# Optimization experiments

Measured on AMD Instinct MI355X. Metric: run time of the kernel, lower is better.

## Reference

```python
import jax, jax.numpy as jnp
import numpy as np

B, H, W, C, HEADS = 4, 64, 64, 512, 8
HD = C // HEADS
L = H * W
BIAS_LEVEL = 0.1
LN_EPS = 1e-5


def _ln(x, g, b):
    mu = jnp.mean(x, axis=-1, keepdims=True)
    var = jnp.var(x, axis=-1, keepdims=True)
    return (x - mu) * jax.lax.rsqrt(var + LN_EPS) * g + b


def setup_inputs() -> dict:
    key = jax.random.key(0)
    ks = jax.random.split(key, 16)
    s = 0.02
    return {
        "x": jax.random.normal(ks[0], (B, L, C), jnp.float32),
        "rpe": jax.random.normal(ks[1], (H, HEADS, W, W), jnp.float32),
        "qkv_w": jax.random.normal(ks[2], (3 * C, C), jnp.float32) * s,
        "proj_w": jax.random.normal(ks[3], (C, C), jnp.float32) * s,
        "proj_b": jnp.zeros((C,), jnp.float32),
        "norm1_w": jnp.ones((C,), jnp.float32),
        "norm1_b": jnp.zeros((C,), jnp.float32),
        "norm2_w": jnp.ones((C,), jnp.float32),
        "norm2_b": jnp.zeros((C,), jnp.float32),
        "fc1_w": jax.random.normal(ks[4], (4 * C, C), jnp.float32) * s,
        "fc1_b": jnp.zeros((4 * C,), jnp.float32),
        "fc2_w": jax.random.normal(ks[5], (C, 4 * C), jnp.float32) * s,
        "fc2_b": jnp.zeros((C,), jnp.float32),
    }


def reference(x, rpe, qkv_w, proj_w, proj_b, norm1_w, norm1_b, norm2_w, norm2_b,
              fc1_w, fc1_b, fc2_w, fc2_b):
    # --- qkv projection ---
    img = _ln(x, norm1_w, norm1_b)
    qkv = (img @ qkv_w.T).reshape(B, L, 3, C)
    q, k, v = qkv[:, :, 0], qkv[:, :, 1], qkv[:, :, 2]

    # idx=0 horizontal windows: each row of the HxW grid is a window of len W.
    def to_win(t):  # (B, L, C) -> (B*H, heads, W, hd)
        return t.reshape(B * H, W, HEADS, HD).transpose(0, 2, 1, 3)

    qw, kw, vw = to_win(q), to_win(k), to_win(v)

    # attention scores + relative position bias (RPE tiled over batch)
    attn = jnp.einsum('whqd,whkd->whqk', qw, kw)
    attn = attn + BIAS_LEVEL * jnp.tile(rpe, (B, 1, 1, 1))

    # magnitude gate M per window
    M = jnp.mean(jnp.abs(attn), axis=(1, 2, 3), keepdims=True)  # (B*H,1,1,1)
    M = M / jnp.max(M)
    M = jnp.maximum(M, 0.5)

    # cosine-based score transform: 1 - cos(pi/2 * l2normalize(attn))
    nrm = jnp.maximum(jnp.linalg.norm(attn, axis=-1, keepdims=True), 1e-12)
    attn = 1.0 - jnp.cos((attn / nrm) * (jnp.pi / 2.0))
    attn = attn * M

    o = jnp.einsum('whqk,whkd->whqd', attn, vw)  # (B*H, heads, W, hd)
    o = o.transpose(0, 2, 1, 3).reshape(B, L, C)

    # residual gating by (1 - M)
    res = (x.reshape(B * H, 1, W, C) * (1.0 - M)).reshape(B, L, C)
    attened = o + res

    attened = attened @ proj_w.T + proj_b
    x1 = x + attened

    h = _ln(x1, norm2_w, norm2_b)
    h = jax.nn.gelu(h @ fc1_w.T + fc1_b, approximate=False)
    h = h @ fc2_w.T + fc2_b
    return x1 + h
```

## Files before the change

### kernel.cpp

```cpp
#include <hip/hip_runtime.h>
#include <hip/hip_bf16.h>
#include <math.h>

typedef unsigned short u16;
typedef __bf16 bf16x8 __attribute__((ext_vector_type(8)));
typedef float f32x4 __attribute__((ext_vector_type(4)));
typedef unsigned short u16x8 __attribute__((ext_vector_type(8)));

typedef const __attribute__((address_space(1))) void* gas_ptr;
typedef __attribute__((address_space(3))) void* las_ptr;

__device__ __forceinline__ float bf2f(u16 u) {
    union { unsigned int i; float f; } x;
    x.i = ((unsigned int)u) << 16;
    return x.f;
}
__device__ __forceinline__ u16 f2bf(float f) {
    __hip_bfloat16 h = __float2bfloat16(f);
    return __builtin_bit_cast(u16, h);
}
__device__ __forceinline__ __bf16 f2bfr(float f) {
    __hip_bfloat16 h = __float2bfloat16(f);
    return __builtin_bit_cast(__bf16, h);
}
__device__ __forceinline__ void load_lds16(const void* g, void* l) {
    __builtin_amdgcn_global_load_lds((gas_ptr)g, (las_ptr)l, 16, 0, 0);
}

__global__ __launch_bounds__(256) void cvt_k(const float* __restrict__ in,
                                             u16* __restrict__ outp) {
    const int i = blockIdx.x * 256 + threadIdx.x;
    const float4 v = ((const float4*)in)[i];
    ushort4 o;
    o.x = f2bf(v.x); o.y = f2bf(v.y); o.z = f2bf(v.z); o.w = f2bf(v.w);
    ((ushort4*)outp)[i] = o;
}

__global__ __launch_bounds__(256) void ln_k(const float* __restrict__ inp,
                                            const float* __restrict__ gw,
                                            const float* __restrict__ gb,
                                            u16* __restrict__ outp) {
    const int row = blockIdx.x, t = threadIdx.x;
    const float2 v = ((const float2*)(inp + (size_t)row * 512))[t];
    float s = v.x + v.y, q = v.x * v.x + v.y * v.y;
    #pragma unroll
    for (int o = 1; o < 64; o <<= 1) {
        s += __shfl_xor(s, o);
        q += __shfl_xor(q, o);
    }
    __shared__ float rs[4], rq[4];
    const int w = t >> 6;
    if ((t & 63) == 0) { rs[w] = s; rq[w] = q; }
    __syncthreads();
    s = rs[0] + rs[1] + rs[2] + rs[3];
    q = rq[0] + rq[1] + rq[2] + rq[3];
    const float mean = s * (1.0f / 512.0f);
    const float var = q * (1.0f / 512.0f) - mean * mean;
    const float rstd = rsqrtf(var + 1e-5f);
    u16* op = outp + (size_t)row * 512;
    op[2 * t]     = f2bf((v.x - mean) * rstd * gw[2 * t]     + gb[2 * t]);
    op[2 * t + 1] = f2bf((v.y - mean) * rstd * gw[2 * t + 1] + gb[2 * t + 1]);
}

template<int EPI>
__global__ __launch_bounds__(256) void gemm_bt(const u16* __restrict__ A,
                                               const u16* __restrict__ W,
                                               const float* __restrict__ bias,
                                               const float* __restrict__ res_f,
                                               void* __restrict__ outp,
                                               int M, int N, int K) {
    __shared__ __bf16 As[2][128 * 32];
    __shared__ __bf16 Bs[2][128 * 32];
    const int t = threadIdx.x;
    const int l = t & 63;
    const int w = t >> 6;
    const int wm = w & 1, wn = w >> 1;
    const int bm = blockIdx.x * 128, bn = blockIdx.y * 128;

    f32x4 acc[4][4] = {};

    auto stage = [&](int buf, int kt) {
        #pragma unroll
        for (int p = 0; p < 2; ++p) {
            const int sb = (p * 256 + t) << 4;
            const int row = sb >> 6;
            const int gl = ((sb >> 4) & 3) ^ (row & 3);
            const int lbase = p * 2048 + w * 512;
            load_lds16(A + (size_t)(bm + row) * K + kt + gl * 8, &As[buf][lbase]);
            load_lds16(W + (size_t)(bn + row) * K + kt + gl * 8, &Bs[buf][lbase]);
        }
    };

    const int nk = K >> 5;
    stage(0, 0);
    __syncthreads();
    for (int s = 0; s < nk; ++s) {
        if (s + 1 < nk) stage((s + 1) & 1, (s + 1) << 5);
        const int buf = s & 1;
        const int r = l & 15, g = l >> 4;
        bf16x8 af[4], bfr[4];
        #pragma unroll
        for (int i = 0; i < 4; ++i) {
            const int ra = wm * 64 + i * 16 + r;
            af[i] = *(const bf16x8*)&As[buf][ra * 32 + ((g ^ (ra & 3)) << 3)];
            const int rb = wn * 64 + i * 16 + r;
            bfr[i] = *(const bf16x8*)&Bs[buf][rb * 32 + ((g ^ (rb & 3)) << 3)];
        }
        #pragma unroll
        for (int i = 0; i < 4; ++i)
            #pragma unroll
            for (int j = 0; j < 4; ++j)
                acc[i][j] = __builtin_amdgcn_mfma_f32_16x16x32_bf16(af[i], bfr[j], acc[i][j], 0, 0, 0);
        __syncthreads();
    }

    #pragma unroll
    for (int i = 0; i < 4; ++i) {
        #pragma unroll
        for (int j = 0; j < 4; ++j) {
            #pragma unroll
            for (int rr = 0; rr < 4; ++rr) {
                const int m = bm + wm * 64 + i * 16 + ((l >> 4) << 2) + rr;
                const int n = bn + wn * 64 + j * 16 + (l & 15);
                float v = acc[i][j][rr];
                const size_t idx = (size_t)m * N + n;
                if (EPI == 0) {
                    ((u16*)outp)[idx] = f2bf(v);
                } else if (EPI == 1) {
                    ((float*)outp)[idx] = v + bias[n] + res_f[idx];
                } else {
                    v += bias[n];
                    v = 0.5f * v * (1.0f + erff(v * 0.70710678118654752f));
                    ((u16*)outp)[idx] = f2bf(v);
                }
            }
        }
    }
}

__global__ __launch_bounds__(256) void attn_k(const u16* __restrict__ qkv,
                                              const float* __restrict__ rpe,
                                              float* __restrict__ Mpart,
                                              u16* __restrict__ Obuf) {
    const int blk = blockIdx.x;
    const int wh = blk >> 3, head = blk & 7;
    const int himg = wh & 63;
    const int t = threadIdx.x, l = t & 63, w = t >> 6;
    __shared__ __bf16 Qs[4096];
    __shared__ __bf16 Ks[4096];
    __shared__ __bf16 Vt[4096];
    __shared__ __bf16 Ps[4096];
    __shared__ float red[4];

    #pragma unroll
    for (int p = 0; p < 2; ++p) {
        const int sb = (p * 256 + t) << 4;
        const int row = sb >> 7;
        const int gl = ((sb >> 4) & 7) ^ (row & 7);
        const size_t gsrc = (size_t)(wh * 64 + row) * 1536 + head * 64 + gl * 8;
        const int lbase = p * 2048 + w * 512;
        load_lds16(qkv + gsrc, &Qs[lbase]);
        load_lds16(qkv + gsrc + 512, &Ks[lbase]);
    }
    {
        const int k = t >> 2, dc = (t & 3) * 16;
        const u16* vr = qkv + (size_t)(wh * 64 + k) * 1536 + 1024 + head * 64 + dc;
        u16x8 v0 = *(const u16x8*)vr;
        u16x8 v1 = *(const u16x8*)(vr + 8);
        const int g = k >> 3, klo = k & 7;
        #pragma unroll
        for (int i = 0; i < 8; ++i) {
            const int d0 = dc + i, d1 = dc + 8 + i;
            Vt[d0 * 64 + ((g ^ (d0 & 7)) << 3) + klo] = __builtin_bit_cast(__bf16, (u16)v0[i]);
            Vt[d1 * 64 + ((g ^ (d1 & 7)) << 3) + klo] = __builtin_bit_cast(__bf16, (u16)v1[i]);
        }
    }
    __syncthreads();

    const int r = l & 15, g4 = l >> 4;
    f32x4 acc[4] = {};
    #pragma unroll
    for (int h = 0; h < 2; ++h) {
        const int rowq = w * 16 + r;
        bf16x8 aq = *(const bf16x8*)&Qs[rowq * 64 + (((h * 4 + g4) ^ (rowq & 7)) << 3)];
        #pragma unroll
        for (int j = 0; j < 4; ++j) {
            const int rowk = j * 16 + r;
            bf16x8 bk = *(const bf16x8*)&Ks[rowk * 64 + (((h * 4 + g4) ^ (rowk & 7)) << 3)];
            acc[j] = __builtin_amdgcn_mfma_f32_16x16x32_bf16(aq, bk, acc[j], 0, 0, 0);
        }
    }

    float v[4][4];
    float asum = 0.f;
    float ss[4] = {0.f, 0.f, 0.f, 0.f};
    const size_t rpe_base = (size_t)(himg * 8 + head) * 4096 + (size_t)(w * 16 + g4 * 4) * 64 + r;
    #pragma unroll
    for (int j = 0; j < 4; ++j) {
        #pragma unroll
        for (int rr = 0; rr < 4; ++rr) {
            const float val = acc[j][rr] + 0.1f * rpe[rpe_base + rr * 64 + j * 16];
            v[j][rr] = val;
            asum += fabsf(val);
            ss[rr] += val * val;
        }
    }
    #pragma unroll
    for (int m = 1; m < 16; m <<= 1) {
        #pragma unroll
        for (int rr = 0; rr < 4; ++rr) ss[rr] += __shfl_xor(ss[rr], m);
    }
    float srev[4];
    #pragma unroll
    for (int rr = 0; rr < 4; ++rr)
        srev[rr] = 0.25f / fmaxf(sqrtf(ss[rr]), 1e-12f);

    #pragma unroll
    for (int j = 0; j < 4; ++j) {
        #pragma unroll
        for (int rr = 0; rr < 4; ++rr) {
            const float pv = 1.0f - __builtin_amdgcn_cosf(v[j][rr] * srev[rr]);
            const int rl = g4 * 4 + rr;
            const int c = j * 16 + r;
            Ps[w * 1024 + rl * 64 + (((c >> 3) ^ (rl & 7)) << 3) + (c & 7)] = f2bfr(pv);
        }
    }

    f32x4 oacc[4] = {};
    #pragma unroll
    for (int ks = 0; ks < 2; ++ks) {
        const int ga = ks * 4 + g4;
        bf16x8 pa = *(const bf16x8*)&Ps[w * 1024 + r * 64 + ((ga ^ (r & 7)) << 3)];
        #pragma unroll
        for (int j = 0; j < 4; ++j) {
            const int d = j * 16 + r;
            bf16x8 vb = *(const bf16x8*)&Vt[d * 64 + ((ga ^ (d & 7)) << 3)];
            oacc[j] = __builtin_amdgcn_mfma_f32_16x16x32_bf16(pa, vb, oacc[j], 0, 0, 0);
        }
    }

    #pragma unroll
    for (int j = 0; j < 4; ++j) {
        #pragma unroll
        for (int rr = 0; rr < 4; ++rr) {
            const int token = wh * 64 + w * 16 + g4 * 4 + rr;
            Obuf[(size_t)token * 512 + head * 64 + j * 16 + r] = f2bf(oacc[j][rr]);
        }
    }

    #pragma unroll
    for (int o = 1; o < 64; o <<= 1) asum += __shfl_xor(asum, o);
    if (l == 0) red[w] = asum;
    __syncthreads();
    if (t == 0) Mpart[blk] = red[0] + red[1] + red[2] + red[3];
}

__global__ __launch_bounds__(256) void mfinal_k(const float* __restrict__ Mpart,
                                                float* __restrict__ M) {
    const int t = threadIdx.x;
    float m = 0.f;
    #pragma unroll
    for (int h = 0; h < 8; ++h) m += Mpart[t * 8 + h];
    m *= (1.0f / 32768.0f);
    float mx = m;
    #pragma unroll
    for (int o = 1; o < 64; o <<= 1) mx = fmaxf(mx, __shfl_xor(mx, o));
    __shared__ float red[4];
    if ((t & 63) == 0) red[t >> 6] = mx;
    __syncthreads();
    mx = fmaxf(fmaxf(red[0], red[1]), fmaxf(red[2], red[3]));
    M[t] = fmaxf(m / mx, 0.5f);
}

__global__ __launch_bounds__(256) void a1_k(const u16* __restrict__ O,
                                            const float* __restrict__ M,
                                            const float* __restrict__ x,
                                            u16* __restrict__ A1) {
    const size_t i8 = ((size_t)blockIdx.x * 256 + threadIdx.x) * 8;
    const float Mw = M[i8 >> 15];
    const float rf = 1.0f - Mw;
    const u16x8 ov = *(const u16x8*)(O + i8);
    const float4 x0 = *(const float4*)(x + i8);
    const float4 x1 = *(const float4*)(x + i8 + 4);
    u16x8 res;
    res[0] = f2bf(bf2f(ov[0]) * Mw + x0.x * rf);
    res[1] = f2bf(bf2f(ov[1]) * Mw + x0.y * rf);
    res[2] = f2bf(bf2f(ov[2]) * Mw + x0.z * rf);
    res[3] = f2bf(bf2f(ov[3]) * Mw + x0.w * rf);
    res[4] = f2bf(bf2f(ov[4]) * Mw + x1.x * rf);
    res[5] = f2bf(bf2f(ov[5]) * Mw + x1.y * rf);
    res[6] = f2bf(bf2f(ov[6]) * Mw + x1.z * rf);
    res[7] = f2bf(bf2f(ov[7]) * Mw + x1.w * rf);
    *(u16x8*)(A1 + i8) = res;
}

extern "C" void kernel_launch(void* const* d_in, const int* in_sizes, int n_in,
                              void* d_out, int out_size, void* d_ws, size_t ws_size,
                              hipStream_t stream) {
    (void)in_sizes; (void)n_in; (void)out_size; (void)ws_size;
    const float* x      = (const float*)d_in[0];
    const float* rpe    = (const float*)d_in[1];
    const float* qkv_w  = (const float*)d_in[2];
    const float* proj_w = (const float*)d_in[3];
    const float* proj_b = (const float*)d_in[4];
    const float* n1w    = (const float*)d_in[5];
    const float* n1b    = (const float*)d_in[6];
    const float* n2w    = (const float*)d_in[7];
    const float* n2b    = (const float*)d_in[8];
    const float* fc1w   = (const float*)d_in[9];
    const float* fc1b   = (const float*)d_in[10];
    const float* fc2w   = (const float*)d_in[11];
    const float* fc2b   = (const float*)d_in[12];
    float* out = (float*)d_out;

    char* ws = (char*)d_ws;
    float* Mpart = (float*)ws;
    float* Mbuf  = (float*)(ws + 8192);
    u16* wqkv  = (u16*)(ws + 16384);
    u16* wproj = (u16*)(ws + 16384 + 1572864);
    u16* wfc1  = (u16*)(ws + 16384 + 2097152);
    u16* wfc2  = (u16*)(ws + 16384 + 4194304);
    u16* bufA  = (u16*)(ws + 6307840);
    char* R    = ws + 23085056;
    u16*   qkvb = (u16*)R;
    u16*   Obuf = (u16*)(R + 50331648);
    u16*   gbuf = (u16*)R;

    cvt_k<<<768, 256, 0, stream>>>(qkv_w, wqkv);
    cvt_k<<<256, 256, 0, stream>>>(proj_w, wproj);
    cvt_k<<<1024, 256, 0, stream>>>(fc1w, wfc1);
    cvt_k<<<1024, 256, 0, stream>>>(fc2w, wfc2);
    ln_k<<<16384, 256, 0, stream>>>(x, n1w, n1b, bufA);
    gemm_bt<0><<<dim3(128, 12), 256, 0, stream>>>(bufA, wqkv, nullptr, nullptr,
                                                  qkvb, 16384, 1536, 512);
    attn_k<<<2048, 256, 0, stream>>>(qkvb, rpe, Mpart, Obuf);
    mfinal_k<<<1, 256, 0, stream>>>(Mpart, Mbuf);
    a1_k<<<4096, 256, 0, stream>>>(Obuf, Mbuf, x, bufA);
    gemm_bt<1><<<dim3(128, 4), 256, 0, stream>>>(bufA, wproj, proj_b, x,
                                                 out, 16384, 512, 512);
    ln_k<<<16384, 256, 0, stream>>>(out, n2w, n2b, bufA);
    gemm_bt<2><<<dim3(128, 16), 256, 0, stream>>>(bufA, wfc1, fc1b, nullptr,
                                                  gbuf, 16384, 2048, 512);
    gemm_bt<1><<<dim3(128, 4), 256, 0, stream>>>(gbuf, wfc2, fc2b, out,
                                                 out, 16384, 512, 2048);
}
```

Measured before the change: 221.1 us.

## Replace GEMM with 8-wave 256-wide tiled kernel using phased LDS prefetch pipeline

Replaces the 128x128, 4-wave GEMM with a 512-thread kernel that computes 128x256 or 256x256 output tiles using K-steps of 64. Loads of A and B into LDS are split into halves and interleaved with MFMA quarters, separated by explicit barriers and vmcnt waits, with raised wave priority around the MFMA sections. The goal is better operand reuse per LDS load and overlap of global-to-LDS traffic with matrix math in all four GEMMs. In exchange it uses more registers and LDS per block, which lowers occupancy. The schedule also depends on hand-tuned wait counts whose correctness has to hold for every stage.

```diff
diff --git a/kernel.cpp b/kernel.cpp
--- a/kernel.cpp
+++ b/kernel.cpp
@@ -26,6 +26,12 @@
 __device__ __forceinline__ void load_lds16(const void* g, void* l) {
     __builtin_amdgcn_global_load_lds((gas_ptr)g, (las_ptr)l, 16, 0, 0);
 }
+__device__ __forceinline__ void phase_bar() {
+    __builtin_amdgcn_sched_barrier(0);
+    __builtin_amdgcn_s_barrier();
+    __builtin_amdgcn_sched_barrier(0);
+}
+#define VMCNT4() asm volatile("s_waitcnt vmcnt(4)" ::: "memory")
 
 __global__ __launch_bounds__(256) void cvt_k(const float* __restrict__ in,
                                              u16* __restrict__ outp) {
@@ -62,66 +68,122 @@
     op[2 * t + 1] = f2bf((v.y - mean) * rstd * gw[2 * t + 1] + gb[2 * t + 1]);
 }
 
-template<int EPI>
-__global__ __launch_bounds__(256) void gemm_bt(const u16* __restrict__ A,
-                                               const u16* __restrict__ W,
-                                               const float* __restrict__ bias,
-                                               const float* __restrict__ res_f,
-                                               void* __restrict__ outp,
-                                               int M, int N, int K) {
-    __shared__ __bf16 As[2][128 * 32];
-    __shared__ __bf16 Bs[2][128 * 32];
+template<int EPI, int M_REP>
+__global__ __launch_bounds__(512, 2) void gemm8(const u16* __restrict__ A,
+                                                const u16* __restrict__ W,
+                                                const float* __restrict__ bias,
+                                                const float* __restrict__ res_f,
+                                                void* __restrict__ outp,
+                                                int M, int N, int K) {
+    constexpr int BM  = M_REP * 32;
+    constexpr int IPQ = M_REP / 4;
+    constexpr int AL  = BM / 128;
+    __shared__ __bf16 As[2][BM * 64];
+    __shared__ __bf16 Bs[2][256 * 64];
     const int t = threadIdx.x;
     const int l = t & 63;
-    const int w = t >> 6;
-    const int wm = w & 1, wn = w >> 1;
-    const int bm = blockIdx.x * 128, bn = blockIdx.y * 128;
-
-    f32x4 acc[4][4] = {};
-
-    auto stage = [&](int buf, int kt) {
-        #pragma unroll
-        for (int p = 0; p < 2; ++p) {
-            const int sb = (p * 256 + t) << 4;
-            const int row = sb >> 6;
-            const int gl = ((sb >> 4) & 3) ^ (row & 3);
-            const int lbase = p * 2048 + w * 512;
-            load_lds16(A + (size_t)(bm + row) * K + kt + gl * 8, &As[buf][lbase]);
-            load_lds16(W + (size_t)(bn + row) * K + kt + gl * 8, &Bs[buf][lbase]);
+    const int wid = t >> 6;
+    const int wm = wid >> 2, wn = wid & 3;
+    const int bm = blockIdx.x * BM, bn = blockIdx.y * 256;
+    const int r = l & 15, g4 = l >> 4;
+    const int nk = K >> 6;
+    const int kmask = nk - 1;
+
+    f32x4 acc[M_REP][4] = {};
+    bf16x8 bfr[4][2];
+    bf16x8 af[IPQ][2];
+
+    auto stageA = [&](int buf, int h, int kt) __attribute__((always_inline)) {
+        const int k0 = (kt & kmask) << 6;
+        #pragma unroll
+        for (int j = 0; j < AL; ++j) {
+            const int gl = h * (BM * 4) + j * 512 + t;
+            const int row = gl >> 3, gc = gl & 7;
+            load_lds16(A + (size_t)(bm + row) * K + k0 + ((gc ^ (row & 7)) << 3),
+                       &As[buf][gl << 3]);
         }
     };
-
-    const int nk = K >> 5;
-    stage(0, 0);
-    __syncthreads();
-    for (int s = 0; s < nk; ++s) {
-        if (s + 1 < nk) stage((s + 1) & 1, (s + 1) << 5);
-        const int buf = s & 1;
-        const int r = l & 15, g = l >> 4;
-        bf16x8 af[4], bfr[4];
-        #pragma unroll
-        for (int i = 0; i < 4; ++i) {
-            const int ra = wm * 64 + i * 16 + r;
-            af[i] = *(const bf16x8*)&As[buf][ra * 32 + ((g ^ (ra & 3)) << 3)];
-            const int rb = wn * 64 + i * 16 + r;
-            bfr[i] = *(const bf16x8*)&Bs[buf][rb * 32 + ((g ^ (rb & 3)) << 3)];
-        }
-        #pragma unroll
-        for (int i = 0; i < 4; ++i)
+    auto stageB = [&](int buf, int h, int kt) __attribute__((always_inline)) {
+        const int k0 = (kt & kmask) << 6;
+        #pragma unroll
+        for (int j = 0; j < 2; ++j) {
+            const int gl = h * 1024 + j * 512 + t;
+            const int row = gl >> 3, gc = gl & 7;
+            load_lds16(W + (size_t)(bn + row) * K + k0 + ((gc ^ (row & 7)) << 3),
+                       &Bs[buf][gl << 3]);
+        }
+    };
+    auto dsB = [&](int buf) __attribute__((always_inline)) {
+        #pragma unroll
+        for (int j = 0; j < 4; ++j) {
+            #pragma unroll
+            for (int ks = 0; ks < 2; ++ks) {
+                const int row = wn * 64 + j * 16 + r;
+                const int gc = ks * 4 + g4;
+                bfr[j][ks] = *(const bf16x8*)&Bs[buf][((row << 3) | (gc ^ (row & 7))) << 3];
+            }
+        }
+    };
+    auto dsA = [&](int buf, int q) __attribute__((always_inline)) {
+        #pragma unroll
+        for (int ii = 0; ii < IPQ; ++ii) {
+            #pragma unroll
+            for (int ks = 0; ks < 2; ++ks) {
+                const int row = wm * (BM / 2) + (q * IPQ + ii) * 16 + r;
+                const int gc = ks * 4 + g4;
+                af[ii][ks] = *(const bf16x8*)&As[buf][((row << 3) | (gc ^ (row & 7))) << 3];
+            }
+        }
+    };
+    auto mfmaQ = [&](int q) __attribute__((always_inline)) {
+        __builtin_amdgcn_s_setprio(1);
+        #pragma unroll
+        for (int ii = 0; ii < IPQ; ++ii)
             #pragma unroll
             for (int j = 0; j < 4; ++j)
-                acc[i][j] = __builtin_amdgcn_mfma_f32_16x16x32_bf16(af[i], bfr[j], acc[i][j], 0, 0, 0);
-        __syncthreads();
-    }
-
-    #pragma unroll
-    for (int i = 0; i < 4; ++i) {
+                #pragma unroll
+                for (int ks = 0; ks < 2; ++ks)
+                    acc[q * IPQ + ii][j] = __builtin_amdgcn_mfma_f32_16x16x32_bf16(
+                        af[ii][ks], bfr[j][ks], acc[q * IPQ + ii][j], 0, 0, 0);
+        __builtin_amdgcn_s_setprio(0);
+    };
+
+    stageA(0, 0, 0); stageA(0, 1, 0);
+    stageB(0, 0, 0); stageB(0, 1, 0);
+    stageB(1, 0, 1); stageB(1, 1, 1);
+    VMCNT4();
+    phase_bar();
+
+    const int niter = nk >> 1;
+    for (int it = 0; it < niter; ++it) {
+        const int Ta = 2 * it;
+        dsB(0); dsA(0, 0);
+        stageA(1, 0, Ta + 1); stageA(1, 1, Ta + 1);
+        phase_bar(); mfmaQ(0); phase_bar();
+        dsA(0, 1); stageB(0, 0, Ta + 2);
+        phase_bar(); mfmaQ(1); phase_bar();
+        dsA(0, 2); stageB(0, 1, Ta + 2);
+        phase_bar(); mfmaQ(2); phase_bar();
+        dsA(0, 3); VMCNT4();
+        phase_bar(); mfmaQ(3); phase_bar();
+        dsB(1); dsA(1, 0); stageA(0, 0, Ta + 2);
+        phase_bar(); mfmaQ(0); phase_bar();
+        dsA(1, 1); stageA(0, 1, Ta + 2);
+        phase_bar(); mfmaQ(1); phase_bar();
+        dsA(1, 2); stageB(1, 0, Ta + 3);
+        phase_bar(); mfmaQ(2); phase_bar();
+        dsA(1, 3); stageB(1, 1, Ta + 3); VMCNT4();
+        phase_bar(); mfmaQ(3); phase_bar();
+    }
+
+    #pragma unroll
+    for (int i = 0; i < M_REP; ++i) {
         #pragma unroll
         for (int j = 0; j < 4; ++j) {
             #pragma unroll
             for (int rr = 0; rr < 4; ++rr) {
-                const int m = bm + wm * 64 + i * 16 + ((l >> 4) << 2) + rr;
-                const int n = bn + wn * 64 + j * 16 + (l & 15);
+                const int m = bm + wm * (BM / 2) + i * 16 + g4 * 4 + rr;
+                const int n = bn + wn * 64 + j * 16 + r;
                 float v = acc[i][j][rr];
                 const size_t idx = (size_t)m * N + n;
                 if (EPI == 0) {
@@ -331,16 +393,16 @@
     cvt_k<<<1024, 256, 0, stream>>>(fc1w, wfc1);
     cvt_k<<<1024, 256, 0, stream>>>(fc2w, wfc2);
     ln_k<<<16384, 256, 0, stream>>>(x, n1w, n1b, bufA);
-    gemm_bt<0><<<dim3(128, 12), 256, 0, stream>>>(bufA, wqkv, nullptr, nullptr,
-                                                  qkvb, 16384, 1536, 512);
+    gemm8<0, 8><<<dim3(64, 6), 512, 0, stream>>>(bufA, wqkv, nullptr, nullptr,
+                                                 qkvb, 16384, 1536, 512);
     attn_k<<<2048, 256, 0, stream>>>(qkvb, rpe, Mpart, Obuf);
     mfinal_k<<<1, 256, 0, stream>>>(Mpart, Mbuf);
     a1_k<<<4096, 256, 0, stream>>>(Obuf, Mbuf, x, bufA);
-    gemm_bt<1><<<dim3(128, 4), 256, 0, stream>>>(bufA, wproj, proj_b, x,
-                                                 out, 16384, 512, 512);
+    gemm8<1, 4><<<dim3(128, 2), 512, 0, stream>>>(bufA, wproj, proj_b, x,
+                                                  out, 16384, 512, 512);
     ln_k<<<16384, 256, 0, stream>>>(out, n2w, n2b, bufA);
-    gemm_bt<2><<<dim3(128, 16), 256, 0, stream>>>(bufA, wfc1, fc1b, nullptr,
-                                                  gbuf, 16384, 2048, 512);
-    gemm_bt<1><<<dim3(128, 4), 256, 0, stream>>>(gbuf, wfc2, fc2b, out,
-                                                 out, 16384, 512, 2048);
-}
+    gemm8<2, 8><<<dim3(64, 8), 512, 0, stream>>>(bufA, wfc1, fc1b, nullptr,
+                                                 gbuf, 16384, 2048, 512);
+    gemm8<1, 4><<<dim3(128, 2), 512, 0, stream>>>(gbuf, wfc2, fc2b, out,
+                                                  out, 16384, 512, 2048);
+}
```

Measured after the change: 229.1 us. 3.6% more time.

## Fuse attention residual gating into proj GEMM loader and store x1 as bf16

Applied to the files above, without the earlier changes.

Removes the standalone a1_k pass by computing M*O + (1-M)*x inside the proj GEMM's A-tile staging, writing the blended bf16 values straight to LDS. The proj output x1 is now stored as bf16 rather than fp32; LN2 reads it as bf16 and the final fc2 GEMM takes it as a bf16 residual. This cuts a full elementwise kernel and its traffic, and halves x1 read/write bytes, at the cost of synchronous register loads instead of async global_load_lds for the A tile and lower precision in the residual path.

```diff
diff --git a/kernel.cpp b/kernel.cpp
--- a/kernel.cpp
+++ b/kernel.cpp
@@ -36,13 +36,21 @@
     ((ushort4*)outp)[i] = o;
 }
 
-__global__ __launch_bounds__(256) void ln_k(const float* __restrict__ inp,
+template<bool BF16IN>
+__global__ __launch_bounds__(256) void ln_k(const void* __restrict__ inp,
                                             const float* __restrict__ gw,
                                             const float* __restrict__ gb,
                                             u16* __restrict__ outp) {
     const int row = blockIdx.x, t = threadIdx.x;
-    const float2 v = ((const float2*)(inp + (size_t)row * 512))[t];
-    float s = v.x + v.y, q = v.x * v.x + v.y * v.y;
+    float v0, v1;
+    if (BF16IN) {
+        const u16* rp = (const u16*)inp + (size_t)row * 512;
+        v0 = bf2f(rp[2 * t]); v1 = bf2f(rp[2 * t + 1]);
+    } else {
+        const float2 v = ((const float2*)((const float*)inp + (size_t)row * 512))[t];
+        v0 = v.x; v1 = v.y;
+    }
+    float s = v0 + v1, q = v0 * v0 + v1 * v1;
     #pragma unroll
     for (int o = 1; o < 64; o <<= 1) {
         s += __shfl_xor(s, o);
@@ -58,17 +66,21 @@
     const float var = q * (1.0f / 512.0f) - mean * mean;
     const float rstd = rsqrtf(var + 1e-5f);
     u16* op = outp + (size_t)row * 512;
-    op[2 * t]     = f2bf((v.x - mean) * rstd * gw[2 * t]     + gb[2 * t]);
-    op[2 * t + 1] = f2bf((v.y - mean) * rstd * gw[2 * t + 1] + gb[2 * t + 1]);
-}
-
-template<int EPI>
+    op[2 * t]     = f2bf((v0 - mean) * rstd * gw[2 * t]     + gb[2 * t]);
+    op[2 * t + 1] = f2bf((v1 - mean) * rstd * gw[2 * t + 1] + gb[2 * t + 1]);
+}
+
+template<int EPI, bool AFUSE>
 __global__ __launch_bounds__(256) void gemm_bt(const u16* __restrict__ A,
                                                const u16* __restrict__ W,
                                                const float* __restrict__ bias,
                                                const float* __restrict__ res_f,
+                                               const u16* __restrict__ res_bf,
                                                void* __restrict__ outp,
-                                               int M, int N, int K) {
+                                               int M, int N, int K,
+                                               const float* __restrict__ aM,
+                                               const u16* __restrict__ aO,
+                                               const float* __restrict__ aX) {
     __shared__ __bf16 As[2][128 * 32];
     __shared__ __bf16 Bs[2][128 * 32];
     const int t = threadIdx.x;
@@ -82,12 +94,33 @@
     auto stage = [&](int buf, int kt) {
         #pragma unroll
         for (int p = 0; p < 2; ++p) {
-            const int sb = (p * 256 + t) << 4;
-            const int row = sb >> 6;
-            const int gl = ((sb >> 4) & 3) ^ (row & 3);
-            const int lbase = p * 2048 + w * 512;
-            load_lds16(A + (size_t)(bm + row) * K + kt + gl * 8, &As[buf][lbase]);
-            load_lds16(W + (size_t)(bn + row) * K + kt + gl * 8, &Bs[buf][lbase]);
+            const int slot = p * 256 + t;
+            const int row = slot >> 2;
+            const int gl = (slot & 3) ^ (row & 3);
+            if (AFUSE) {
+                const int grow = bm + row;
+                const size_t gidx = (size_t)grow * K + kt + gl * 8;
+                const float Mw = aM[grow >> 6];
+                const float rf = 1.0f - Mw;
+                const u16x8 ov = *(const u16x8*)(aO + gidx);
+                const float4 x0 = *(const float4*)(aX + gidx);
+                const float4 x1 = *(const float4*)(aX + gidx + 4);
+                bf16x8 val;
+                val[0] = f2bfr(Mw * bf2f(ov[0]) + rf * x0.x);
+                val[1] = f2bfr(Mw * bf2f(ov[1]) + rf * x0.y);
+                val[2] = f2bfr(Mw * bf2f(ov[2]) + rf * x0.z);
+                val[3] = f2bfr(Mw * bf2f(ov[3]) + rf * x0.w);
+                val[4] = f2bfr(Mw * bf2f(ov[4]) + rf * x1.x);
+                val[5] = f2bfr(Mw * bf2f(ov[5]) + rf * x1.y);
+                val[6] = f2bfr(Mw * bf2f(ov[6]) + rf * x1.z);
+                val[7] = f2bfr(Mw * bf2f(ov[7]) + rf * x1.w);
+                *(bf16x8*)&As[buf][slot * 8] = val;
+            } else {
+                load_lds16(A + (size_t)(bm + row) * K + kt + gl * 8,
+                           &As[buf][p * 2048 + w * 512]);
+            }
+            load_lds16(W + (size_t)(bn + row) * K + kt + gl * 8,
+                       &Bs[buf][p * 2048 + w * 512]);
         }
     };
 
@@ -127,11 +160,13 @@
                 if (EPI == 0) {
                     ((u16*)outp)[idx] = f2bf(v);
                 } else if (EPI == 1) {
-                    ((float*)outp)[idx] = v + bias[n] + res_f[idx];
-                } else {
+                    ((u16*)outp)[idx] = f2bf(v + bias[n] + res_f[idx]);
+                } else if (EPI == 2) {
                     v += bias[n];
                     v = 0.5f * v * (1.0f + erff(v * 0.70710678118654752f));
                     ((u16*)outp)[idx] = f2bf(v);
+                } else {
+                    ((float*)outp)[idx] = v + bias[n] + bf2f(res_bf[idx]);
                 }
             }
         }
@@ -270,28 +305,6 @@
     __syncthreads();
     mx = fmaxf(fmaxf(red[0], red[1]), fmaxf(red[2], red[3]));
     M[t] = fmaxf(m / mx, 0.5f);
-}
-
-__global__ __launch_bounds__(256) void a1_k(const u16* __restrict__ O,
-                                            const float* __restrict__ M,
-                                            const float* __restrict__ x,
-                                            u16* __restrict__ A1) {
-    const size_t i8 = ((size_t)blockIdx.x * 256 + threadIdx.x) * 8;
-    const float Mw = M[i8 >> 15];
-    const float rf = 1.0f - Mw;
-    const u16x8 ov = *(const u16x8*)(O + i8);
-    const float4 x0 = *(const float4*)(x + i8);
-    const float4 x1 = *(const float4*)(x + i8 + 4);
-    u16x8 res;
-    res[0] = f2bf(bf2f(ov[0]) * Mw + x0.x * rf);
-    res[1] = f2bf(bf2f(ov[1]) * Mw + x0.y * rf);
-    res[2] = f2bf(bf2f(ov[2]) * Mw + x0.z * rf);
-    res[3] = f2bf(bf2f(ov[3]) * Mw + x0.w * rf);
-    res[4] = f2bf(bf2f(ov[4]) * Mw + x1.x * rf);
-    res[5] = f2bf(bf2f(ov[5]) * Mw + x1.y * rf);
-    res[6] = f2bf(bf2f(ov[6]) * Mw + x1.z * rf);
-    res[7] = f2bf(bf2f(ov[7]) * Mw + x1.w * rf);
-    *(u16x8*)(A1 + i8) = res;
 }
 
 extern "C" void kernel_launch(void* const* d_in, const int* in_sizes, int n_in,
@@ -321,7 +334,8 @@
     u16* wfc1  = (u16*)(ws + 16384 + 2097152);
     u16* wfc2  = (u16*)(ws + 16384 + 4194304);
     u16* bufA  = (u16*)(ws + 6307840);
-    char* R    = ws + 23085056;
+    u16* bufB  = (u16*)(ws + 23085056);
+    char* R    = ws + 39862272;
     u16*   qkvb = (u16*)R;
     u16*   Obuf = (u16*)(R + 50331648);
     u16*   gbuf = (u16*)R;
@@ -330,17 +344,20 @@
     cvt_k<<<256, 256, 0, stream>>>(proj_w, wproj);
     cvt_k<<<1024, 256, 0, stream>>>(fc1w, wfc1);
     cvt_k<<<1024, 256, 0, stream>>>(fc2w, wfc2);
-    ln_k<<<16384, 256, 0, stream>>>(x, n1w, n1b, bufA);
-    gemm_bt<0><<<dim3(128, 12), 256, 0, stream>>>(bufA, wqkv, nullptr, nullptr,
-                                                  qkvb, 16384, 1536, 512);
+    ln_k<false><<<16384, 256, 0, stream>>>(x, n1w, n1b, bufA);
+    gemm_bt<0, false><<<dim3(128, 12), 256, 0, stream>>>(
+        bufA, wqkv, nullptr, nullptr, nullptr, qkvb, 16384, 1536, 512,
+        nullptr, nullptr, nullptr);
     attn_k<<<2048, 256, 0, stream>>>(qkvb, rpe, Mpart, Obuf);
     mfinal_k<<<1, 256, 0, stream>>>(Mpart, Mbuf);
-    a1_k<<<4096, 256, 0, stream>>>(Obuf, Mbuf, x, bufA);
-    gemm_bt<1><<<dim3(128, 4), 256, 0, stream>>>(bufA, wproj, proj_b, x,
-                                                 out, 16384, 512, 512);
-    ln_k<<<16384, 256, 0, stream>>>(out, n2w, n2b, bufA);
-    gemm_bt<2><<<dim3(128, 16), 256, 0, stream>>>(bufA, wfc1, fc1b, nullptr,
-                                                  gbuf, 16384, 2048, 512);
-    gemm_bt<1><<<dim3(128, 4), 256, 0, stream>>>(gbuf, wfc2, fc2b, out,
-                                                 out, 16384, 512, 2048);
-}
+    gemm_bt<1, true><<<dim3(128, 4), 256, 0, stream>>>(
+        nullptr, wproj, proj_b, x, nullptr, bufA, 16384, 512, 512,
+        Mbuf, Obuf, x);
+    ln_k<true><<<16384, 256, 0, stream>>>(bufA, n2w, n2b, bufB);
+    gemm_bt<2, false><<<dim3(128, 16), 256, 0, stream>>>(
+        bufB, wfc1, fc1b, nullptr, nullptr, gbuf, 16384, 2048, 512,
+        nullptr, nullptr, nullptr);
+    gemm_bt<3, false><<<dim3(128, 4), 256, 0, stream>>>(
+        gbuf, wfc2, fc2b, nullptr, bufA, out, 16384, 512, 2048,
+        nullptr, nullptr, nullptr);
+}
```

Result: faster. 213.6 us (-3.4%).
